# Kernel tuning notes

Measured on AMD Instinct MI355X. Metric: run time of the kernel, lower is better.

The kernel has to match this reference:

```python
import jax, jax.numpy as jnp
import numpy as np

B, C, H, W = 2, 256, 64, 64
HEADS = 4
K = 64  # max attendable keys per query
GROUPS = 32
EPS = 1e-6


def group_norm(x, scale, bias):
    b, c, h, w = x.shape
    xg = x.reshape(b, GROUPS, c // GROUPS, h, w)
    mean = xg.mean(axis=(2, 3, 4), keepdims=True)
    var = xg.var(axis=(2, 3, 4), keepdims=True)
    xn = ((xg - mean) * jax.lax.rsqrt(var + EPS)).reshape(b, c, h, w)
    return xn * scale[None, :, None, None] + bias[None, :, None, None]


def conv1x1(x, w, b):
    return jnp.einsum('oc,bchw->bohw', w, x) + b[None, :, None, None]


def setup_inputs() -> dict:
    key = jax.random.key(0)
    ks = jax.random.split(key, 8)
    x = jax.random.normal(ks[0], (B, C, H, W), dtype=jnp.float32)
    valid_indices_mask = jax.random.randint(ks[1], (H * W, K), 0, 2, dtype=jnp.int32)
    attendable_indices = jax.random.randint(ks[2], (H * W, K), 0, H * W, dtype=jnp.int32)
    s = 0.02
    wq = jax.random.normal(ks[3], (C, C), dtype=jnp.float32) * s
    wk = jax.random.normal(ks[4], (C, C), dtype=jnp.float32) * s
    wv = jax.random.normal(ks[5], (C, C), dtype=jnp.float32) * s
    wo = jax.random.normal(ks[6], (C, C), dtype=jnp.float32) * s
    return {
        'x': x,
        'valid_indices_mask': valid_indices_mask,
        'attendable_indices': attendable_indices,
        'gn_scale': jnp.ones((C,), jnp.float32),
        'gn_bias': jnp.zeros((C,), jnp.float32),
        'wq': wq, 'bq': jnp.zeros((C,), jnp.float32),
        'wk': wk, 'bk': jnp.zeros((C,), jnp.float32),
        'wv': wv, 'bv': jnp.zeros((C,), jnp.float32),
        'wo': wo, 'bo': jnp.zeros((C,), jnp.float32),
    }


def reference(x, valid_indices_mask, attendable_indices, gn_scale, gn_bias,
              wq, bq, wk, bk, wv, bv, wo, bo):
    b, c, h, w = x.shape
    nq = h * w
    d = c // HEADS
    h_ = group_norm(x, gn_scale, gn_bias)
    q = conv1x1(h_, wq, bq).reshape(b, HEADS, d, nq)
    k = conv1x1(h_, wk, bk).reshape(b, HEADS, d, nq)
    v = conv1x1(h_, wv, bv).reshape(b, HEADS, d, nq)
    # gather per-query attendable keys/values: [b, heads, nq, K, d]
    kt = k.transpose(0, 1, 3, 2)  # [b, heads, nv, d]
    vt = v.transpose(0, 1, 3, 2)
    ak = kt[:, :, attendable_indices]  # [b, heads, nq, K, d]
    av = vt[:, :, attendable_indices]
    # beta = 1 (no 1/sqrt(d) scaling in the sparse path, per original code)
    logits = jnp.einsum('bhqkc,bhcq->bhqk', ak, q)
    neg = jnp.where(valid_indices_mask == 0, -jnp.inf, 0.0).astype(logits.dtype)
    logits = logits + neg[None, None, :, :]
    weights = jax.nn.softmax(logits, axis=-1)
    attn = jnp.einsum('bhqk,bhqkc->bhqc', weights, av)  # [b, heads, nq, d]
    attn = attn.transpose(0, 3, 1, 2).reshape(b, c, h, w)
    out = x + conv1x1(attn, wo, bo)
    return out
```

## Files before the change

### kernel.cpp

```cpp
#include <hip/hip_runtime.h>
#include <math.h>

typedef unsigned int uint;
typedef unsigned short ushort;
typedef __attribute__((ext_vector_type(8))) short bf16x8;
typedef __attribute__((ext_vector_type(4))) float f32x4;

#define LSTR 40

__device__ __forceinline__ float bf2f(ushort u) { return __uint_as_float(((uint)u) << 16); }
__device__ __forceinline__ ushort f2bf(float f) {
    uint u = __float_as_uint(f);
    return (ushort)((u + 0x7fffu + ((u >> 16) & 1u)) >> 16);
}

__global__ __launch_bounds__(256) void gn_part_k(const float* __restrict__ x,
                                                 float* __restrict__ stats) {
    const int bg = blockIdx.x >> 2, part = blockIdx.x & 3;
    const float4* base = (const float4*)(x + (size_t)bg * 32768 + part * 8192);
    float s = 0.f, ss = 0.f;
    for (int i = threadIdx.x; i < 2048; i += 256) {
        float4 v = base[i];
        s  += v.x + v.y + v.z + v.w;
        ss += v.x*v.x + v.y*v.y + v.z*v.z + v.w*v.w;
    }
    #pragma unroll
    for (int o = 32; o; o >>= 1) { s += __shfl_xor(s, o); ss += __shfl_xor(ss, o); }
    if ((threadIdx.x & 63) == 0) {
        atomicAdd(&stats[bg * 2],     s);
        atomicAdd(&stats[bg * 2 + 1], ss);
    }
}

__global__ __launch_bounds__(256) void gn_apply_t_k(const float* __restrict__ x,
        const float* __restrict__ stats, const float* __restrict__ sc,
        const float* __restrict__ bi, ushort* __restrict__ hT) {
    const int n0 = blockIdx.x * 64, c0 = blockIdx.y * 64, b = blockIdx.z;
    __shared__ ushort tile[64][65];
    const int t = threadIdx.x;
    #pragma unroll
    for (int it = 0; it < 4; ++it) {
        const int r = (t >> 4) + it * 16, col4 = t & 15;
        const int c = c0 + r, bg = b * 32 + (c >> 3);
        const float S = stats[bg * 2], SS = stats[bg * 2 + 1];
        const float mean = S * (1.f / 32768.f);
        const float var  = SS * (1.f / 32768.f) - mean * mean;
        const float a  = rsqrtf(var + 1e-6f) * sc[c];
        const float bb = bi[c] - mean * a;
        float4 v = *(const float4*)(x + ((size_t)(b * 256 + c)) * 4096 + n0 + col4 * 4);
        tile[r][col4*4 + 0] = f2bf(v.x * a + bb);
        tile[r][col4*4 + 1] = f2bf(v.y * a + bb);
        tile[r][col4*4 + 2] = f2bf(v.z * a + bb);
        tile[r][col4*4 + 3] = f2bf(v.w * a + bb);
    }
    __syncthreads();
    #pragma unroll
    for (int it = 0; it < 2; ++it) {
        const int nr = (t >> 3) + it * 32, c8 = t & 7;
        uint4 st;
        ushort e0 = tile[c8*8+0][nr], e1 = tile[c8*8+1][nr];
        ushort e2 = tile[c8*8+2][nr], e3 = tile[c8*8+3][nr];
        ushort e4 = tile[c8*8+4][nr], e5 = tile[c8*8+5][nr];
        ushort e6 = tile[c8*8+6][nr], e7 = tile[c8*8+7][nr];
        st.x = (uint)e0 | ((uint)e1 << 16);
        st.y = (uint)e2 | ((uint)e3 << 16);
        st.z = (uint)e4 | ((uint)e5 << 16);
        st.w = (uint)e6 | ((uint)e7 << 16);
        *(uint4*)(hT + ((size_t)b * 4096 + n0 + nr) * 256 + c0 + c8 * 8) = st;
    }
}

__global__ __launch_bounds__(256) void wprep_k(
        const float* __restrict__ wq, const float* __restrict__ wk,
        const float* __restrict__ wv, const float* __restrict__ wo,
        const float* __restrict__ bq, const float* __restrict__ bk,
        const float* __restrict__ bv,
        ushort* __restrict__ wqkv, ushort* __restrict__ wo_p,
        float* __restrict__ bqkv) {
    const int i = blockIdx.x * 256 + threadIdx.x;
    if (i < 196608) {
        const int o = i >> 8, k = i & 255;
        const float* W = (o < 256) ? wq : ((o < 512) ? wk : wv);
        wqkv[i] = f2bf(W[(o & 255) * 256 + k]);
    } else if (i < 262144) {
        const int j = i - 196608;
        const int o = j >> 8, kp = j & 255;
        const int h = kp >> 6, d = kp & 63;
        wo_p[j] = f2bf(wo[o * 256 + d * 4 + h]);
    } else if (i < 262912) {
        const int o = i - 262144;
        bqkv[o] = (o < 256) ? bq[o] : ((o < 512) ? bk[o - 256] : bv[o - 512]);
    }
}

__global__ __launch_bounds__(256) void qkv_gemm_k(
        const ushort* __restrict__ Wqkv, const float* __restrict__ bqkv,
        const ushort* __restrict__ hT, float* __restrict__ qf,
        ushort* __restrict__ kvb) {
    const int nt = blockIdx.x, mt = blockIdx.y, b = blockIdx.z;
    __shared__ ushort As[128 * LSTR];
    __shared__ ushort Bs[64 * LSTR];
    const int t = threadIdx.x;
    const int wave = t >> 6, ln = t & 63;
    const int wm = wave >> 1, wn = wave & 1;
    f32x4 acc[4][2] = {};
    const ushort* Ag = Wqkv + (size_t)(mt * 128) * 256;
    const ushort* Bg = hT + ((size_t)b * 4096 + nt * 64) * 256;
    const int srow = t >> 2, sc8 = (t & 3) * 8;
    const int fr = ln & 15, kA = (ln >> 4) * 8;

    for (int k0 = 0; k0 < 256; k0 += 32) {
        *(uint4*)&As[srow * LSTR + sc8]        = *(const uint4*)&Ag[(size_t)srow * 256 + k0 + sc8];
        *(uint4*)&As[(srow + 64) * LSTR + sc8] = *(const uint4*)&Ag[(size_t)(srow + 64) * 256 + k0 + sc8];
        *(uint4*)&Bs[srow * LSTR + sc8]        = *(const uint4*)&Bg[(size_t)srow * 256 + k0 + sc8];
        __syncthreads();
        bf16x8 af[4], bfr[2];
        #pragma unroll
        for (int m = 0; m < 4; ++m) af[m]  = *(bf16x8*)&As[(wm * 64 + m * 16 + fr) * LSTR + kA];
        #pragma unroll
        for (int n = 0; n < 2; ++n) bfr[n] = *(bf16x8*)&Bs[(wn * 32 + n * 16 + fr) * LSTR + kA];
        #pragma unroll
        for (int m = 0; m < 4; ++m)
            #pragma unroll
            for (int n = 0; n < 2; ++n)
                acc[m][n] = __builtin_amdgcn_mfma_f32_16x16x32_bf16(af[m], bfr[n], acc[m][n], 0, 0, 0);
        __syncthreads();
    }
    const int colb = nt * 64 + wn * 32 + fr;
    const int rowb = mt * 128 + wm * 64;
    #pragma unroll
    for (int m = 0; m < 4; ++m) {
        const int o0 = rowb + m * 16 + ((ln >> 4) << 2);
        const int proj = o0 >> 8;
        const int head = (o0 >> 6) & 3;
        const int d0 = o0 & 63;
        const float4 bi4 = *(const float4*)&bqkv[o0];
        if (proj == 0) {
            float* obase = qf + ((size_t)(b * 4 + head) * 4096) * 64 + d0;
            #pragma unroll
            for (int n = 0; n < 2; ++n) {
                const int nn = colb + n * 16;
                f32x4 a = acc[m][n];
                float4 st = { a[0] + bi4.x, a[1] + bi4.y, a[2] + bi4.z, a[3] + bi4.w };
                *(float4*)&obase[(size_t)nn * 64] = st;
            }
        } else {
            ushort* obase = kvb + ((size_t)(proj - 1) * 8 + (b * 4 + head)) * (4096 * 64) + d0;
            #pragma unroll
            for (int n = 0; n < 2; ++n) {
                const int nn = colb + n * 16;
                f32x4 a = acc[m][n];
                uint2 st;
                st.x = (uint)f2bf(a[0] + bi4.x) | ((uint)f2bf(a[1] + bi4.y) << 16);
                st.y = (uint)f2bf(a[2] + bi4.z) | ((uint)f2bf(a[3] + bi4.w) << 16);
                *(uint2*)&obase[(size_t)nn * 64] = st;
            }
        }
    }
}

__global__ __launch_bounds__(256) void attn_k(
        const float* __restrict__ qf, const ushort* __restrict__ kb,
        const ushort* __restrict__ vb, const int* __restrict__ aidx,
        const int* __restrict__ vmask, ushort* __restrict__ attnb) {
    const int bh = blockIdx.x & 7;
    const int q4 = blockIdx.x >> 3;
    const int wave = threadIdx.x >> 6, ln = threadIdx.x & 63;
    const int n = q4 * 4 + wave;
    const ushort* kbase = kb + (size_t)bh * (4096 * 64);
    const ushort* vbase = vb + (size_t)bh * (4096 * 64);
    const int idx = aidx[n * 64 + ln];
    const int msk = vmask[n * 64 + ln];

    const int nu = __builtin_amdgcn_readfirstlane(n);
    const float4* __restrict__ qrow4 =
        (const float4*)(qf + ((size_t)bh * 4096 + nu) * 64);

    const uint4* krow = (const uint4*)(kbase + (size_t)idx * 64);
    float d0 = 0.f, d1 = 0.f, d2 = 0.f, d3 = 0.f;
    #pragma unroll
    for (int c = 0; c < 8; ++c) {
        uint4 u = krow[c];
        float4 qa = qrow4[c * 2];
        float4 qb = qrow4[c * 2 + 1];
        d0 += __uint_as_float(u.x << 16)         * qa.x;
        d1 += __uint_as_float(u.x & 0xffff0000u) * qa.y;
        d2 += __uint_as_float(u.y << 16)         * qa.z;
        d3 += __uint_as_float(u.y & 0xffff0000u) * qa.w;
        d0 += __uint_as_float(u.z << 16)         * qb.x;
        d1 += __uint_as_float(u.z & 0xffff0000u) * qb.y;
        d2 += __uint_as_float(u.w << 16)         * qb.z;
        d3 += __uint_as_float(u.w & 0xffff0000u) * qb.w;
    }
    const float dot = (d0 + d1) + (d2 + d3);
    float mx = msk ? dot : -1e30f;
    #pragma unroll
    for (int o = 32; o; o >>= 1) mx = fmaxf(mx, __shfl_xor(mx, o));
    const float e = msk ? __expf(dot - mx) : 0.f;
    float s = e;
    #pragma unroll
    for (int o = 32; o; o >>= 1) s += __shfl_xor(s, o);
    const float wgt = e / s;

    __shared__ uint2 pw[4][64];
    pw[wave][ln] = make_uint2((uint)idx << 7, __float_as_uint(wgt));

    const int p = ln >> 4, d4 = ln & 15;
    const uint2* pwp = &pw[wave][p];
    const char* vb2 = (const char*)(vbase + d4 * 4);
    float a0 = 0.f, a1 = 0.f, a2 = 0.f, a3 = 0.f;
    #pragma unroll
    for (int k = 0; k < 64; k += 4) {
        const uint2 iw = pwp[k];
        const uint2 u = *(const uint2*)(vb2 + iw.x);
        const float sw = __uint_as_float(iw.y);
        a0 += sw * __uint_as_float(u.x << 16);
        a1 += sw * __uint_as_float(u.x & 0xffff0000u);
        a2 += sw * __uint_as_float(u.y << 16);
        a3 += sw * __uint_as_float(u.y & 0xffff0000u);
    }
    #pragma unroll
    for (int o = 16; o <= 32; o <<= 1) {
        a0 += __shfl_xor(a0, o); a1 += __shfl_xor(a1, o);
        a2 += __shfl_xor(a2, o); a3 += __shfl_xor(a3, o);
    }
    if (p == 0) {
        const int b = bh >> 2, h = bh & 3;
        uint2 st;
        st.x = (uint)f2bf(a0) | ((uint)f2bf(a1) << 16);
        st.y = (uint)f2bf(a2) | ((uint)f2bf(a3) << 16);
        *(uint2*)(attnb + ((size_t)b * 4096 + n) * 256 + h * 64 + d4 * 4) = st;
    }
}

__global__ __launch_bounds__(256) void out_gemm_k(
        const ushort* __restrict__ wo_p, const float* __restrict__ bo,
        const ushort* __restrict__ attnb, const float* __restrict__ x,
        float* __restrict__ outp) {
    const int nt = blockIdx.x, mt = blockIdx.y, b = blockIdx.z;
    __shared__ ushort As[64 * LSTR];
    __shared__ ushort Bs[64 * LSTR];
    const int t = threadIdx.x;
    const int wave = t >> 6, ln = t & 63;
    const int wm = wave >> 1, wn = wave & 1;
    f32x4 acc[2][2] = {};
    const ushort* Ag = wo_p + (size_t)(mt * 64) * 256;
    const ushort* Bg = attnb + ((size_t)b * 4096 + nt * 64) * 256;
    const int srow = t >> 2, sc8 = (t & 3) * 8;
    const int fr = ln & 15, kA = (ln >> 4) * 8;

    for (int k0 = 0; k0 < 256; k0 += 32) {
        *(uint4*)&As[srow * LSTR + sc8] = *(const uint4*)&Ag[(size_t)srow * 256 + k0 + sc8];
        *(uint4*)&Bs[srow * LSTR + sc8] = *(const uint4*)&Bg[(size_t)srow * 256 + k0 + sc8];
        __syncthreads();
        bf16x8 af[2], bfr[2];
        #pragma unroll
        for (int m = 0; m < 2; ++m) af[m]  = *(bf16x8*)&As[(wm * 32 + m * 16 + fr) * LSTR + kA];
        #pragma unroll
        for (int n = 0; n < 2; ++n) bfr[n] = *(bf16x8*)&Bs[(wn * 32 + n * 16 + fr) * LSTR + kA];
        #pragma unroll
        for (int m = 0; m < 2; ++m)
            #pragma unroll
            for (int n = 0; n < 2; ++n)
                acc[m][n] = __builtin_amdgcn_mfma_f32_16x16x32_bf16(af[m], bfr[n], acc[m][n], 0, 0, 0);
        __syncthreads();
    }
    const int colb = nt * 64 + wn * 32 + fr;
    const int rowb = mt * 64 + wm * 32;
    #pragma unroll
    for (int m = 0; m < 2; ++m) {
        const int o0 = rowb + m * 16 + ((ln >> 4) << 2);
        const float4 bi4 = *(const float4*)&bo[o0];
        const float* bip = (const float*)&bi4;
        #pragma unroll
        for (int n = 0; n < 2; ++n) {
            const int nn = colb + n * 16;
            #pragma unroll
            for (int r = 0; r < 4; ++r) {
                const size_t a = ((size_t)(b * 256 + o0 + r)) * 4096 + nn;
                outp[a] = acc[m][n][r] + bip[r] + x[a];
            }
        }
    }
}

extern "C" void kernel_launch(void* const* d_in, const int* in_sizes, int n_in,
                              void* d_out, int out_size, void* d_ws, size_t ws_size,
                              hipStream_t stream) {
    const float* x     = (const float*)d_in[0];
    const int*   vmask = (const int*)d_in[1];
    const int*   aidx  = (const int*)d_in[2];
    const float* gsc   = (const float*)d_in[3];
    const float* gbi   = (const float*)d_in[4];
    const float* wq    = (const float*)d_in[5];
    const float* bq    = (const float*)d_in[6];
    const float* wk    = (const float*)d_in[7];
    const float* bk    = (const float*)d_in[8];
    const float* wv    = (const float*)d_in[9];
    const float* bv    = (const float*)d_in[10];
    const float* wo    = (const float*)d_in[11];
    const float* bo    = (const float*)d_in[12];
    float* outp = (float*)d_out;

    char* w = (char*)d_ws;
    float*  stats = (float*)w;
    ushort* wqkv  = (ushort*)(w + 1024);
    ushort* wo_p  = (ushort*)(w + 394240);
    float*  bqkv  = (float*)(w + 525312);
    ushort* hT    = (ushort*)(w + 528384);
    float*  qf    = (float*)(w + 4722688);
    ushort* kvb   = (ushort*)(w + 13111296);
    ushort* attnb = (ushort*)(w + 21499904);

    ushort* kbuf = kvb;
    ushort* vbuf = kvb + 2097152;

    hipMemsetAsync(stats, 0, 512, stream);
    hipLaunchKernelGGL(gn_part_k,    dim3(256),        dim3(256), 0, stream, x, stats);
    hipLaunchKernelGGL(wprep_k,      dim3(1027),       dim3(256), 0, stream,
                       wq, wk, wv, wo, bq, bk, bv, wqkv, wo_p, bqkv);
    hipLaunchKernelGGL(gn_apply_t_k, dim3(64, 4, 2),   dim3(256), 0, stream,
                       x, stats, gsc, gbi, hT);
    hipLaunchKernelGGL(qkv_gemm_k,   dim3(64, 6, 2),   dim3(256), 0, stream,
                       wqkv, bqkv, hT, qf, kvb);
    hipLaunchKernelGGL(attn_k,       dim3(8192),       dim3(256), 0, stream,
                       qf, kbuf, vbuf, aidx, vmask, attnb);
    hipLaunchKernelGGL(out_gemm_k,   dim3(64, 4, 2),   dim3(256), 0, stream,
                       wo_p, bo, attnb, x, outp);
}
```

Measured before the change: 169.3 us.

## Store Q in bf16, process two queries per wave, merge prep kernels

Q is now written as bf16 alongside K and V instead of fp32, which halves Q traffic and lets the dot product decode bf16 pairs. The attention kernel handles two queries per wave, interleaving their gathers and reductions to give more memory-level parallelism, and launches half as many blocks. The group-norm statistics and weight-prep kernels are merged into one launch. Rounding Q to bf16 lowers precision of the logits, which matters here because there is no 1/sqrt(d) scaling.

```diff
diff --git a/kernel.cpp b/kernel.cpp
--- a/kernel.cpp
+++ b/kernel.cpp
@@ -9,26 +9,51 @@
 #define LSTR 40
 
 __device__ __forceinline__ float bf2f(ushort u) { return __uint_as_float(((uint)u) << 16); }
+__device__ __forceinline__ float blo(uint v) { return __uint_as_float(v << 16); }
+__device__ __forceinline__ float bhi(uint v) { return __uint_as_float(v & 0xffff0000u); }
 __device__ __forceinline__ ushort f2bf(float f) {
     uint u = __float_as_uint(f);
     return (ushort)((u + 0x7fffu + ((u >> 16) & 1u)) >> 16);
 }
 
-__global__ __launch_bounds__(256) void gn_part_k(const float* __restrict__ x,
-                                                 float* __restrict__ stats) {
-    const int bg = blockIdx.x >> 2, part = blockIdx.x & 3;
-    const float4* base = (const float4*)(x + (size_t)bg * 32768 + part * 8192);
-    float s = 0.f, ss = 0.f;
-    for (int i = threadIdx.x; i < 2048; i += 256) {
-        float4 v = base[i];
-        s  += v.x + v.y + v.z + v.w;
-        ss += v.x*v.x + v.y*v.y + v.z*v.z + v.w*v.w;
-    }
-    #pragma unroll
-    for (int o = 32; o; o >>= 1) { s += __shfl_xor(s, o); ss += __shfl_xor(ss, o); }
-    if ((threadIdx.x & 63) == 0) {
-        atomicAdd(&stats[bg * 2],     s);
-        atomicAdd(&stats[bg * 2 + 1], ss);
+__global__ __launch_bounds__(256) void prep_k(const float* __restrict__ x,
+        float* __restrict__ stats,
+        const float* __restrict__ wq, const float* __restrict__ wk,
+        const float* __restrict__ wv, const float* __restrict__ wo,
+        const float* __restrict__ bq, const float* __restrict__ bk,
+        const float* __restrict__ bv,
+        ushort* __restrict__ wqkv, ushort* __restrict__ wo_p,
+        float* __restrict__ bqkv) {
+    if (blockIdx.x < 256) {
+        const int bg = blockIdx.x >> 2, part = blockIdx.x & 3;
+        const float4* base = (const float4*)(x + (size_t)bg * 32768 + part * 8192);
+        float s = 0.f, ss = 0.f;
+        for (int i = threadIdx.x; i < 2048; i += 256) {
+            float4 v = base[i];
+            s  += v.x + v.y + v.z + v.w;
+            ss += v.x*v.x + v.y*v.y + v.z*v.z + v.w*v.w;
+        }
+        #pragma unroll
+        for (int o = 32; o; o >>= 1) { s += __shfl_xor(s, o); ss += __shfl_xor(ss, o); }
+        if ((threadIdx.x & 63) == 0) {
+            atomicAdd(&stats[bg * 2],     s);
+            atomicAdd(&stats[bg * 2 + 1], ss);
+        }
+        return;
+    }
+    const int i = (blockIdx.x - 256) * 256 + threadIdx.x;
+    if (i < 196608) {
+        const int o = i >> 8, k = i & 255;
+        const float* W = (o < 256) ? wq : ((o < 512) ? wk : wv);
+        wqkv[i] = f2bf(W[(o & 255) * 256 + k]);
+    } else if (i < 262144) {
+        const int j = i - 196608;
+        const int o = j >> 8, kp = j & 255;
+        const int h = kp >> 6, d = kp & 63;
+        wo_p[j] = f2bf(wo[o * 256 + d * 4 + h]);
+    } else if (i < 262912) {
+        const int o = i - 262144;
+        bqkv[o] = (o < 256) ? bq[o] : ((o < 512) ? bk[o - 256] : bv[o - 512]);
     }
 }
 
@@ -70,33 +95,9 @@
     }
 }
 
-__global__ __launch_bounds__(256) void wprep_k(
-        const float* __restrict__ wq, const float* __restrict__ wk,
-        const float* __restrict__ wv, const float* __restrict__ wo,
-        const float* __restrict__ bq, const float* __restrict__ bk,
-        const float* __restrict__ bv,
-        ushort* __restrict__ wqkv, ushort* __restrict__ wo_p,
-        float* __restrict__ bqkv) {
-    const int i = blockIdx.x * 256 + threadIdx.x;
-    if (i < 196608) {
-        const int o = i >> 8, k = i & 255;
-        const float* W = (o < 256) ? wq : ((o < 512) ? wk : wv);
-        wqkv[i] = f2bf(W[(o & 255) * 256 + k]);
-    } else if (i < 262144) {
-        const int j = i - 196608;
-        const int o = j >> 8, kp = j & 255;
-        const int h = kp >> 6, d = kp & 63;
-        wo_p[j] = f2bf(wo[o * 256 + d * 4 + h]);
-    } else if (i < 262912) {
-        const int o = i - 262144;
-        bqkv[o] = (o < 256) ? bq[o] : ((o < 512) ? bk[o - 256] : bv[o - 512]);
-    }
-}
-
 __global__ __launch_bounds__(256) void qkv_gemm_k(
         const ushort* __restrict__ Wqkv, const float* __restrict__ bqkv,
-        const ushort* __restrict__ hT, float* __restrict__ qf,
-        ushort* __restrict__ kvb) {
+        const ushort* __restrict__ hT, ushort* __restrict__ qkvb) {
     const int nt = blockIdx.x, mt = blockIdx.y, b = blockIdx.z;
     __shared__ ushort As[128 * LSTR];
     __shared__ ushort Bs[64 * LSTR];
@@ -135,101 +136,106 @@
         const int head = (o0 >> 6) & 3;
         const int d0 = o0 & 63;
         const float4 bi4 = *(const float4*)&bqkv[o0];
-        if (proj == 0) {
-            float* obase = qf + ((size_t)(b * 4 + head) * 4096) * 64 + d0;
-            #pragma unroll
-            for (int n = 0; n < 2; ++n) {
-                const int nn = colb + n * 16;
-                f32x4 a = acc[m][n];
-                float4 st = { a[0] + bi4.x, a[1] + bi4.y, a[2] + bi4.z, a[3] + bi4.w };
-                *(float4*)&obase[(size_t)nn * 64] = st;
-            }
-        } else {
-            ushort* obase = kvb + ((size_t)(proj - 1) * 8 + (b * 4 + head)) * (4096 * 64) + d0;
-            #pragma unroll
-            for (int n = 0; n < 2; ++n) {
-                const int nn = colb + n * 16;
-                f32x4 a = acc[m][n];
-                uint2 st;
-                st.x = (uint)f2bf(a[0] + bi4.x) | ((uint)f2bf(a[1] + bi4.y) << 16);
-                st.y = (uint)f2bf(a[2] + bi4.z) | ((uint)f2bf(a[3] + bi4.w) << 16);
-                *(uint2*)&obase[(size_t)nn * 64] = st;
-            }
+        ushort* obase = qkvb + ((size_t)proj * 8 + (b * 4 + head)) * (4096 * 64) + d0;
+        #pragma unroll
+        for (int n = 0; n < 2; ++n) {
+            const int nn = colb + n * 16;
+            f32x4 a = acc[m][n];
+            uint2 st;
+            st.x = (uint)f2bf(a[0] + bi4.x) | ((uint)f2bf(a[1] + bi4.y) << 16);
+            st.y = (uint)f2bf(a[2] + bi4.z) | ((uint)f2bf(a[3] + bi4.w) << 16);
+            *(uint2*)&obase[(size_t)nn * 64] = st;
         }
     }
 }
 
 __global__ __launch_bounds__(256) void attn_k(
-        const float* __restrict__ qf, const ushort* __restrict__ kb,
+        const ushort* __restrict__ qb, const ushort* __restrict__ kb,
         const ushort* __restrict__ vb, const int* __restrict__ aidx,
         const int* __restrict__ vmask, ushort* __restrict__ attnb) {
     const int bh = blockIdx.x & 7;
-    const int q4 = blockIdx.x >> 3;
+    const int q8 = blockIdx.x >> 3;
     const int wave = threadIdx.x >> 6, ln = threadIdx.x & 63;
-    const int n = q4 * 4 + wave;
+    const int n0 = q8 * 8 + wave * 2;
     const ushort* kbase = kb + (size_t)bh * (4096 * 64);
     const ushort* vbase = vb + (size_t)bh * (4096 * 64);
-    const int idx = aidx[n * 64 + ln];
-    const int msk = vmask[n * 64 + ln];
-
-    const int nu = __builtin_amdgcn_readfirstlane(n);
-    const float4* __restrict__ qrow4 =
-        (const float4*)(qf + ((size_t)bh * 4096 + nu) * 64);
-
-    const uint4* krow = (const uint4*)(kbase + (size_t)idx * 64);
-    float d0 = 0.f, d1 = 0.f, d2 = 0.f, d3 = 0.f;
+
+    const int nu = __builtin_amdgcn_readfirstlane(n0);
+    const uint4* __restrict__ q0p = (const uint4*)(qb + ((size_t)bh * 4096 + nu) * 64);
+    const uint4* __restrict__ q1p = (const uint4*)(qb + ((size_t)bh * 4096 + nu + 1) * 64);
+
+    const int idx0 = aidx[n0 * 64 + ln],       msk0 = vmask[n0 * 64 + ln];
+    const int idx1 = aidx[(n0 + 1) * 64 + ln], msk1 = vmask[(n0 + 1) * 64 + ln];
+
+    const uint4* kr0 = (const uint4*)(kbase + (size_t)idx0 * 64);
+    const uint4* kr1 = (const uint4*)(kbase + (size_t)idx1 * 64);
+    float p0a = 0.f, p0b = 0.f, p1a = 0.f, p1b = 0.f;
     #pragma unroll
     for (int c = 0; c < 8; ++c) {
-        uint4 u = krow[c];
-        float4 qa = qrow4[c * 2];
-        float4 qb = qrow4[c * 2 + 1];
-        d0 += __uint_as_float(u.x << 16)         * qa.x;
-        d1 += __uint_as_float(u.x & 0xffff0000u) * qa.y;
-        d2 += __uint_as_float(u.y << 16)         * qa.z;
-        d3 += __uint_as_float(u.y & 0xffff0000u) * qa.w;
-        d0 += __uint_as_float(u.z << 16)         * qb.x;
-        d1 += __uint_as_float(u.z & 0xffff0000u) * qb.y;
-        d2 += __uint_as_float(u.w << 16)         * qb.z;
-        d3 += __uint_as_float(u.w & 0xffff0000u) * qb.w;
-    }
-    const float dot = (d0 + d1) + (d2 + d3);
-    float mx = msk ? dot : -1e30f;
-    #pragma unroll
-    for (int o = 32; o; o >>= 1) mx = fmaxf(mx, __shfl_xor(mx, o));
-    const float e = msk ? __expf(dot - mx) : 0.f;
-    float s = e;
-    #pragma unroll
-    for (int o = 32; o; o >>= 1) s += __shfl_xor(s, o);
-    const float wgt = e / s;
-
-    __shared__ uint2 pw[4][64];
-    pw[wave][ln] = make_uint2((uint)idx << 7, __float_as_uint(wgt));
+        const uint4 u0 = kr0[c], u1 = kr1[c];
+        const uint4 qa = q0p[c], qc = q1p[c];
+        p0a += blo(u0.x) * blo(qa.x) + blo(u0.y) * blo(qa.y)
+             + blo(u0.z) * blo(qa.z) + blo(u0.w) * blo(qa.w);
+        p0b += bhi(u0.x) * bhi(qa.x) + bhi(u0.y) * bhi(qa.y)
+             + bhi(u0.z) * bhi(qa.z) + bhi(u0.w) * bhi(qa.w);
+        p1a += blo(u1.x) * blo(qc.x) + blo(u1.y) * blo(qc.y)
+             + blo(u1.z) * blo(qc.z) + blo(u1.w) * blo(qc.w);
+        p1b += bhi(u1.x) * bhi(qc.x) + bhi(u1.y) * bhi(qc.y)
+             + bhi(u1.z) * bhi(qc.z) + bhi(u1.w) * bhi(qc.w);
+    }
+    const float dot0 = p0a + p0b, dot1 = p1a + p1b;
+    float mx0 = msk0 ? dot0 : -1e30f, mx1 = msk1 ? dot1 : -1e30f;
+    #pragma unroll
+    for (int o = 32; o; o >>= 1) {
+        mx0 = fmaxf(mx0, __shfl_xor(mx0, o));
+        mx1 = fmaxf(mx1, __shfl_xor(mx1, o));
+    }
+    const float e0 = msk0 ? __expf(dot0 - mx0) : 0.f;
+    const float e1 = msk1 ? __expf(dot1 - mx1) : 0.f;
+    float s0 = e0, s1 = e1;
+    #pragma unroll
+    for (int o = 32; o; o >>= 1) { s0 += __shfl_xor(s0, o); s1 += __shfl_xor(s1, o); }
+    const float w0 = e0 / s0, w1 = e1 / s1;
+
+    __shared__ uint2 pw[4][2][64];
+    pw[wave][0][ln] = make_uint2((uint)idx0 << 7, __float_as_uint(w0));
+    pw[wave][1][ln] = make_uint2((uint)idx1 << 7, __float_as_uint(w1));
 
     const int p = ln >> 4, d4 = ln & 15;
-    const uint2* pwp = &pw[wave][p];
+    const uint2* pw0 = &pw[wave][0][p];
+    const uint2* pw1 = &pw[wave][1][p];
     const char* vb2 = (const char*)(vbase + d4 * 4);
     float a0 = 0.f, a1 = 0.f, a2 = 0.f, a3 = 0.f;
+    float b0 = 0.f, b1 = 0.f, b2 = 0.f, b3 = 0.f;
     #pragma unroll
     for (int k = 0; k < 64; k += 4) {
-        const uint2 iw = pwp[k];
-        const uint2 u = *(const uint2*)(vb2 + iw.x);
-        const float sw = __uint_as_float(iw.y);
-        a0 += sw * __uint_as_float(u.x << 16);
-        a1 += sw * __uint_as_float(u.x & 0xffff0000u);
-        a2 += sw * __uint_as_float(u.y << 16);
-        a3 += sw * __uint_as_float(u.y & 0xffff0000u);
+        const uint2 iw0 = pw0[k];
+        const uint2 iw1 = pw1[k];
+        const uint2 u0 = *(const uint2*)(vb2 + iw0.x);
+        const uint2 u1 = *(const uint2*)(vb2 + iw1.x);
+        const float sw0 = __uint_as_float(iw0.y);
+        const float sw1 = __uint_as_float(iw1.y);
+        a0 += sw0 * blo(u0.x); a1 += sw0 * bhi(u0.x);
+        a2 += sw0 * blo(u0.y); a3 += sw0 * bhi(u0.y);
+        b0 += sw1 * blo(u1.x); b1 += sw1 * bhi(u1.x);
+        b2 += sw1 * blo(u1.y); b3 += sw1 * bhi(u1.y);
     }
     #pragma unroll
     for (int o = 16; o <= 32; o <<= 1) {
         a0 += __shfl_xor(a0, o); a1 += __shfl_xor(a1, o);
         a2 += __shfl_xor(a2, o); a3 += __shfl_xor(a3, o);
+        b0 += __shfl_xor(b0, o); b1 += __shfl_xor(b1, o);
+        b2 += __shfl_xor(b2, o); b3 += __shfl_xor(b3, o);
     }
     if (p == 0) {
         const int b = bh >> 2, h = bh & 3;
-        uint2 st;
-        st.x = (uint)f2bf(a0) | ((uint)f2bf(a1) << 16);
-        st.y = (uint)f2bf(a2) | ((uint)f2bf(a3) << 16);
-        *(uint2*)(attnb + ((size_t)b * 4096 + n) * 256 + h * 64 + d4 * 4) = st;
+        uint2 st0, st1;
+        st0.x = (uint)f2bf(a0) | ((uint)f2bf(a1) << 16);
+        st0.y = (uint)f2bf(a2) | ((uint)f2bf(a3) << 16);
+        st1.x = (uint)f2bf(b0) | ((uint)f2bf(b1) << 16);
+        st1.y = (uint)f2bf(b2) | ((uint)f2bf(b3) << 16);
+        *(uint2*)(attnb + ((size_t)b * 4096 + n0)     * 256 + h * 64 + d4 * 4) = st0;
+        *(uint2*)(attnb + ((size_t)b * 4096 + n0 + 1) * 256 + h * 64 + d4 * 4) = st1;
     }
 }
 
@@ -308,23 +314,22 @@
     ushort* wo_p  = (ushort*)(w + 394240);
     float*  bqkv  = (float*)(w + 525312);
     ushort* hT    = (ushort*)(w + 528384);
-    float*  qf    = (float*)(w + 4722688);
-    ushort* kvb   = (ushort*)(w + 13111296);
-    ushort* attnb = (ushort*)(w + 21499904);
-
-    ushort* kbuf = kvb;
-    ushort* vbuf = kvb + 2097152;
+    ushort* qkvb  = (ushort*)(w + 4722688);
+    ushort* attnb = (ushort*)(w + 17305600);
+
+    ushort* qbuf = qkvb;
+    ushort* kbuf = qkvb + 2097152;
+    ushort* vbuf = qkvb + 4194304;
 
     hipMemsetAsync(stats, 0, 512, stream);
-    hipLaunchKernelGGL(gn_part_k,    dim3(256),        dim3(256), 0, stream, x, stats);
-    hipLaunchKernelGGL(wprep_k,      dim3(1027),       dim3(256), 0, stream,
-                       wq, wk, wv, wo, bq, bk, bv, wqkv, wo_p, bqkv);
+    hipLaunchKernelGGL(prep_k,       dim3(1283),       dim3(256), 0, stream,
+                       x, stats, wq, wk, wv, wo, bq, bk, bv, wqkv, wo_p, bqkv);
     hipLaunchKernelGGL(gn_apply_t_k, dim3(64, 4, 2),   dim3(256), 0, stream,
                        x, stats, gsc, gbi, hT);
     hipLaunchKernelGGL(qkv_gemm_k,   dim3(64, 6, 2),   dim3(256), 0, stream,
-                       wqkv, bqkv, hT, qf, kvb);
-    hipLaunchKernelGGL(attn_k,       dim3(8192),       dim3(256), 0, stream,
-                       qf, kbuf, vbuf, aidx, vmask, attnb);
+                       wqkv, bqkv, hT, qkvb);
+    hipLaunchKernelGGL(attn_k,       dim3(4096),       dim3(256), 0, stream,
+                       qbuf, kbuf, vbuf, aidx, vmask, attnb);
     hipLaunchKernelGGL(out_gemm_k,   dim3(64, 4, 2),   dim3(256), 0, stream,
                        wo_p, bo, attnb, x, outp);
 }
```

Result: slower. 181.2 us (+7.0%).

## Store Q as bf16, merge prep kernels, batch V gathers in attention

Applied to the files above, without the earlier changes.

Q is now written by the QKV GEMM as bf16 in a unified qkv buffer instead of fp32. This halves Q write and read traffic and makes the attention Q loads match the K row format. The GroupNorm-stats and weight-prep kernels are fused into one launch to save a kernel launch. The V gather loop is restructured to issue all 16 index loads and gathers before accumulating, which raises memory-level parallelism at the cost of more registers. Q precision drops to bf16, so accuracy is slightly lower.

```diff
diff --git a/kernel.cpp b/kernel.cpp
--- a/kernel.cpp
+++ b/kernel.cpp
@@ -9,26 +9,51 @@
 #define LSTR 40
 
 __device__ __forceinline__ float bf2f(ushort u) { return __uint_as_float(((uint)u) << 16); }
+__device__ __forceinline__ float blo(uint v) { return __uint_as_float(v << 16); }
+__device__ __forceinline__ float bhi(uint v) { return __uint_as_float(v & 0xffff0000u); }
 __device__ __forceinline__ ushort f2bf(float f) {
     uint u = __float_as_uint(f);
     return (ushort)((u + 0x7fffu + ((u >> 16) & 1u)) >> 16);
 }
 
-__global__ __launch_bounds__(256) void gn_part_k(const float* __restrict__ x,
-                                                 float* __restrict__ stats) {
-    const int bg = blockIdx.x >> 2, part = blockIdx.x & 3;
-    const float4* base = (const float4*)(x + (size_t)bg * 32768 + part * 8192);
-    float s = 0.f, ss = 0.f;
-    for (int i = threadIdx.x; i < 2048; i += 256) {
-        float4 v = base[i];
-        s  += v.x + v.y + v.z + v.w;
-        ss += v.x*v.x + v.y*v.y + v.z*v.z + v.w*v.w;
-    }
-    #pragma unroll
-    for (int o = 32; o; o >>= 1) { s += __shfl_xor(s, o); ss += __shfl_xor(ss, o); }
-    if ((threadIdx.x & 63) == 0) {
-        atomicAdd(&stats[bg * 2],     s);
-        atomicAdd(&stats[bg * 2 + 1], ss);
+__global__ __launch_bounds__(256) void prep_k(const float* __restrict__ x,
+        float* __restrict__ stats,
+        const float* __restrict__ wq, const float* __restrict__ wk,
+        const float* __restrict__ wv, const float* __restrict__ wo,
+        const float* __restrict__ bq, const float* __restrict__ bk,
+        const float* __restrict__ bv,
+        ushort* __restrict__ wqkv, ushort* __restrict__ wo_p,
+        float* __restrict__ bqkv) {
+    if (blockIdx.x < 256) {
+        const int bg = blockIdx.x >> 2, part = blockIdx.x & 3;
+        const float4* base = (const float4*)(x + (size_t)bg * 32768 + part * 8192);
+        float s = 0.f, ss = 0.f;
+        for (int i = threadIdx.x; i < 2048; i += 256) {
+            float4 v = base[i];
+            s  += v.x + v.y + v.z + v.w;
+            ss += v.x*v.x + v.y*v.y + v.z*v.z + v.w*v.w;
+        }
+        #pragma unroll
+        for (int o = 32; o; o >>= 1) { s += __shfl_xor(s, o); ss += __shfl_xor(ss, o); }
+        if ((threadIdx.x & 63) == 0) {
+            atomicAdd(&stats[bg * 2],     s);
+            atomicAdd(&stats[bg * 2 + 1], ss);
+        }
+        return;
+    }
+    const int i = (blockIdx.x - 256) * 256 + threadIdx.x;
+    if (i < 196608) {
+        const int o = i >> 8, k = i & 255;
+        const float* W = (o < 256) ? wq : ((o < 512) ? wk : wv);
+        wqkv[i] = f2bf(W[(o & 255) * 256 + k]);
+    } else if (i < 262144) {
+        const int j = i - 196608;
+        const int o = j >> 8, kp = j & 255;
+        const int h = kp >> 6, d = kp & 63;
+        wo_p[j] = f2bf(wo[o * 256 + d * 4 + h]);
+    } else if (i < 262912) {
+        const int o = i - 262144;
+        bqkv[o] = (o < 256) ? bq[o] : ((o < 512) ? bk[o - 256] : bv[o - 512]);
     }
 }
 
@@ -70,33 +95,9 @@
     }
 }
 
-__global__ __launch_bounds__(256) void wprep_k(
-        const float* __restrict__ wq, const float* __restrict__ wk,
-        const float* __restrict__ wv, const float* __restrict__ wo,
-        const float* __restrict__ bq, const float* __restrict__ bk,
-        const float* __restrict__ bv,
-        ushort* __restrict__ wqkv, ushort* __restrict__ wo_p,
-        float* __restrict__ bqkv) {
-    const int i = blockIdx.x * 256 + threadIdx.x;
-    if (i < 196608) {
-        const int o = i >> 8, k = i & 255;
-        const float* W = (o < 256) ? wq : ((o < 512) ? wk : wv);
-        wqkv[i] = f2bf(W[(o & 255) * 256 + k]);
-    } else if (i < 262144) {
-        const int j = i - 196608;
-        const int o = j >> 8, kp = j & 255;
-        const int h = kp >> 6, d = kp & 63;
-        wo_p[j] = f2bf(wo[o * 256 + d * 4 + h]);
-    } else if (i < 262912) {
-        const int o = i - 262144;
-        bqkv[o] = (o < 256) ? bq[o] : ((o < 512) ? bk[o - 256] : bv[o - 512]);
-    }
-}
-
 __global__ __launch_bounds__(256) void qkv_gemm_k(
         const ushort* __restrict__ Wqkv, const float* __restrict__ bqkv,
-        const ushort* __restrict__ hT, float* __restrict__ qf,
-        ushort* __restrict__ kvb) {
+        const ushort* __restrict__ hT, ushort* __restrict__ qkvb) {
     const int nt = blockIdx.x, mt = blockIdx.y, b = blockIdx.z;
     __shared__ ushort As[128 * LSTR];
     __shared__ ushort Bs[64 * LSTR];
@@ -135,32 +136,21 @@
         const int head = (o0 >> 6) & 3;
         const int d0 = o0 & 63;
         const float4 bi4 = *(const float4*)&bqkv[o0];
-        if (proj == 0) {
-            float* obase = qf + ((size_t)(b * 4 + head) * 4096) * 64 + d0;
-            #pragma unroll
-            for (int n = 0; n < 2; ++n) {
-                const int nn = colb + n * 16;
-                f32x4 a = acc[m][n];
-                float4 st = { a[0] + bi4.x, a[1] + bi4.y, a[2] + bi4.z, a[3] + bi4.w };
-                *(float4*)&obase[(size_t)nn * 64] = st;
-            }
-        } else {
-            ushort* obase = kvb + ((size_t)(proj - 1) * 8 + (b * 4 + head)) * (4096 * 64) + d0;
-            #pragma unroll
-            for (int n = 0; n < 2; ++n) {
-                const int nn = colb + n * 16;
-                f32x4 a = acc[m][n];
-                uint2 st;
-                st.x = (uint)f2bf(a[0] + bi4.x) | ((uint)f2bf(a[1] + bi4.y) << 16);
-                st.y = (uint)f2bf(a[2] + bi4.z) | ((uint)f2bf(a[3] + bi4.w) << 16);
-                *(uint2*)&obase[(size_t)nn * 64] = st;
-            }
+        ushort* obase = qkvb + ((size_t)proj * 8 + (b * 4 + head)) * (4096 * 64) + d0;
+        #pragma unroll
+        for (int n = 0; n < 2; ++n) {
+            const int nn = colb + n * 16;
+            f32x4 a = acc[m][n];
+            uint2 st;
+            st.x = (uint)f2bf(a[0] + bi4.x) | ((uint)f2bf(a[1] + bi4.y) << 16);
+            st.y = (uint)f2bf(a[2] + bi4.z) | ((uint)f2bf(a[3] + bi4.w) << 16);
+            *(uint2*)&obase[(size_t)nn * 64] = st;
         }
     }
 }
 
 __global__ __launch_bounds__(256) void attn_k(
-        const float* __restrict__ qf, const ushort* __restrict__ kb,
+        const ushort* __restrict__ qb, const ushort* __restrict__ kb,
         const ushort* __restrict__ vb, const int* __restrict__ aidx,
         const int* __restrict__ vmask, ushort* __restrict__ attnb) {
     const int bh = blockIdx.x & 7;
@@ -169,30 +159,25 @@
     const int n = q4 * 4 + wave;
     const ushort* kbase = kb + (size_t)bh * (4096 * 64);
     const ushort* vbase = vb + (size_t)bh * (4096 * 64);
+
+    const int nu = __builtin_amdgcn_readfirstlane(n);
+    const uint4* __restrict__ qp = (const uint4*)(qb + ((size_t)bh * 4096 + nu) * 64);
+
     const int idx = aidx[n * 64 + ln];
     const int msk = vmask[n * 64 + ln];
 
-    const int nu = __builtin_amdgcn_readfirstlane(n);
-    const float4* __restrict__ qrow4 =
-        (const float4*)(qf + ((size_t)bh * 4096 + nu) * 64);
-
-    const uint4* krow = (const uint4*)(kbase + (size_t)idx * 64);
-    float d0 = 0.f, d1 = 0.f, d2 = 0.f, d3 = 0.f;
+    const uint4* kr = (const uint4*)(kbase + (size_t)idx * 64);
+    float p0 = 0.f, p1 = 0.f;
     #pragma unroll
     for (int c = 0; c < 8; ++c) {
-        uint4 u = krow[c];
-        float4 qa = qrow4[c * 2];
-        float4 qb = qrow4[c * 2 + 1];
-        d0 += __uint_as_float(u.x << 16)         * qa.x;
-        d1 += __uint_as_float(u.x & 0xffff0000u) * qa.y;
-        d2 += __uint_as_float(u.y << 16)         * qa.z;
-        d3 += __uint_as_float(u.y & 0xffff0000u) * qa.w;
-        d0 += __uint_as_float(u.z << 16)         * qb.x;
-        d1 += __uint_as_float(u.z & 0xffff0000u) * qb.y;
-        d2 += __uint_as_float(u.w << 16)         * qb.z;
-        d3 += __uint_as_float(u.w & 0xffff0000u) * qb.w;
-    }
-    const float dot = (d0 + d1) + (d2 + d3);
+        const uint4 u = kr[c];
+        const uint4 qa = qp[c];
+        p0 += blo(u.x) * blo(qa.x) + blo(u.y) * blo(qa.y)
+            + blo(u.z) * blo(qa.z) + blo(u.w) * blo(qa.w);
+        p1 += bhi(u.x) * bhi(qa.x) + bhi(u.y) * bhi(qa.y)
+            + bhi(u.z) * bhi(qa.z) + bhi(u.w) * bhi(qa.w);
+    }
+    const float dot = p0 + p1;
     float mx = msk ? dot : -1e30f;
     #pragma unroll
     for (int o = 32; o; o >>= 1) mx = fmaxf(mx, __shfl_xor(mx, o));
@@ -208,16 +193,20 @@
     const int p = ln >> 4, d4 = ln & 15;
     const uint2* pwp = &pw[wave][p];
     const char* vb2 = (const char*)(vbase + d4 * 4);
+
+    uint2 iw[16];
+    #pragma unroll
+    for (int k = 0; k < 16; ++k) iw[k] = pwp[k * 4];
+    uint2 vv[16];
+    #pragma unroll
+    for (int k = 0; k < 16; ++k)
+        vv[k] = *(const uint2*)(vb2 + iw[k].x);
     float a0 = 0.f, a1 = 0.f, a2 = 0.f, a3 = 0.f;
     #pragma unroll
-    for (int k = 0; k < 64; k += 4) {
-        const uint2 iw = pwp[k];
-        const uint2 u = *(const uint2*)(vb2 + iw.x);
-        const float sw = __uint_as_float(iw.y);
-        a0 += sw * __uint_as_float(u.x << 16);
-        a1 += sw * __uint_as_float(u.x & 0xffff0000u);
-        a2 += sw * __uint_as_float(u.y << 16);
-        a3 += sw * __uint_as_float(u.y & 0xffff0000u);
+    for (int k = 0; k < 16; ++k) {
+        const float sw = __uint_as_float(iw[k].y);
+        a0 += sw * blo(vv[k].x); a1 += sw * bhi(vv[k].x);
+        a2 += sw * blo(vv[k].y); a3 += sw * bhi(vv[k].y);
     }
     #pragma unroll
     for (int o = 16; o <= 32; o <<= 1) {
@@ -308,23 +297,22 @@
     ushort* wo_p  = (ushort*)(w + 394240);
     float*  bqkv  = (float*)(w + 525312);
     ushort* hT    = (ushort*)(w + 528384);
-    float*  qf    = (float*)(w + 4722688);
-    ushort* kvb   = (ushort*)(w + 13111296);
-    ushort* attnb = (ushort*)(w + 21499904);
-
-    ushort* kbuf = kvb;
-    ushort* vbuf = kvb + 2097152;
+    ushort* qkvb  = (ushort*)(w + 4722688);
+    ushort* attnb = (ushort*)(w + 17305600);
+
+    ushort* qbuf = qkvb;
+    ushort* kbuf = qkvb + 2097152;
+    ushort* vbuf = qkvb + 4194304;
 
     hipMemsetAsync(stats, 0, 512, stream);
-    hipLaunchKernelGGL(gn_part_k,    dim3(256),        dim3(256), 0, stream, x, stats);
-    hipLaunchKernelGGL(wprep_k,      dim3(1027),       dim3(256), 0, stream,
-                       wq, wk, wv, wo, bq, bk, bv, wqkv, wo_p, bqkv);
+    hipLaunchKernelGGL(prep_k,       dim3(1283),       dim3(256), 0, stream,
+                       x, stats, wq, wk, wv, wo, bq, bk, bv, wqkv, wo_p, bqkv);
     hipLaunchKernelGGL(gn_apply_t_k, dim3(64, 4, 2),   dim3(256), 0, stream,
                        x, stats, gsc, gbi, hT);
     hipLaunchKernelGGL(qkv_gemm_k,   dim3(64, 6, 2),   dim3(256), 0, stream,
-                       wqkv, bqkv, hT, qf, kvb);
+                       wqkv, bqkv, hT, qkvb);
     hipLaunchKernelGGL(attn_k,       dim3(8192),       dim3(256), 0, stream,
-                       qf, kbuf, vbuf, aidx, vmask, attnb);
+                       qbuf, kbuf, vbuf, aidx, vmask, attnb);
     hipLaunchKernelGGL(out_gemm_k,   dim3(64, 4, 2),   dim3(256), 0, stream,
                        wo_p, bo, attnb, x, outp);
 }
```

Measured after the change: 168.6 us. About the same (-0.4%).
